# Performance work log

Hardware: AMD Instinct MI355X
Metric: run time of the kernel (lower is better)

## Reference

```python
import jax, jax.numpy as jnp
import numpy as np

N, NFEAT, NHID, NCLASS, NHEADS = 4096, 512, 64, 40, 8
ALPHA = 0.2
NEG = -9e15


def setup_inputs() -> dict:
    key = jax.random.key(0)
    ks = jax.random.split(key, 6)
    x = jax.random.normal(ks[0], (N, NFEAT), dtype=jnp.float32)
    adj = jax.random.randint(ks[1], (2, N, N), 0, 2, dtype=jnp.int32)
    # Xavier-ish scaled params
    W1 = jax.random.normal(ks[2], (NHEADS, NFEAT, NHID), dtype=jnp.float32) * (1.0 / np.sqrt(NFEAT))
    a1 = jax.random.normal(ks[3], (NHEADS, 2, NHID), dtype=jnp.float32) * (1.0 / np.sqrt(2 * NHID))
    Wo = jax.random.normal(ks[4], (NHEADS * NHID, NCLASS), dtype=jnp.float32) * (1.0 / np.sqrt(NHEADS * NHID))
    ao = jax.random.normal(ks[5], (2, NCLASS), dtype=jnp.float32) * (1.0 / np.sqrt(2 * NCLASS))
    return {"x": x, "adj": adj, "W1": W1, "a1": a1, "Wo": Wo, "ao": ao}


def _gat_layer(h, adj_mask, W, a_src, a_dst, concat):
    # h: [N,F]; W: [...,F,F']; a_src/a_dst: [...,F']
    if W.ndim == 3:  # multi-head: [H,F,F']
        Wh = jnp.einsum('nf,hfd->hnd', h, W)              # [H,N,F']
        f1 = jnp.einsum('hnd,hd->hn', Wh, a_src)           # [H,N]
        f2 = jnp.einsum('hnd,hd->hn', Wh, a_dst)
        e = jax.nn.leaky_relu(f1[:, :, None] + f2[:, None, :], ALPHA)  # [H,N,N]
        e = jnp.where(adj_mask[None], e, NEG)
        att = jax.nn.softmax(e, axis=-1)
        out = jnp.einsum('hnm,hmd->hnd', att, Wh)          # [H,N,F']
    else:
        Wh = h @ W                                         # [N,F']
        f1 = Wh @ a_src
        f2 = Wh @ a_dst
        e = jax.nn.leaky_relu(f1[:, None] + f2[None, :], ALPHA)
        e = jnp.where(adj_mask, e, NEG)
        att = jax.nn.softmax(e, axis=-1)
        out = att @ Wh
    return jax.nn.elu(out) if concat else out


def reference(x, adj, W1, a1, Wo, ao):
    adj1 = adj[1] > 0
    adj0 = adj[0] > 0
    # layer 1: NHEADS heads, concat=True
    h = _gat_layer(x, adj1, W1, a1[:, 0], a1[:, 1], concat=True)   # [H,N,NHID]
    h = jnp.transpose(h, (1, 0, 2)).reshape(x.shape[0], -1)        # [N, H*NHID]
    # output layer: concat=False, then outer ELU + log_softmax
    out = _gat_layer(h, adj0, Wo, ao[0], ao[1], concat=False)      # [N, NCLASS]
    out = jax.nn.elu(out)
    return jax.nn.log_softmax(out, axis=1)
```

## Files before the change

### kernel.cpp

```cpp
#include <hip/hip_runtime.h>
#include <hip/hip_bf16.h>

#define N      4096
#define NFEAT  512
#define NHID   64
#define NHEADS 8
#define NCLASS 40
#define ALPHA  0.2f
#define LOG2E  1.44269504f

typedef unsigned short u16;
typedef unsigned int   u32;
typedef __attribute__((ext_vector_type(8))) short bf16x8;
typedef __attribute__((ext_vector_type(4))) float f32x4;

__device__ __forceinline__ float b2f(u16 u) {
    return __uint_as_float(((u32)u) << 16);
}
__device__ __forceinline__ u32 rnd_hi(float f) {
    u32 u = __float_as_uint(f);
    return u + 0x7FFFu + ((u >> 16) & 1u);
}
__device__ __forceinline__ u32 pk2(float lo, float hi) {
    __hip_bfloat162 h = __float22bfloat162_rn(make_float2(lo, hi));
    return *(u32*)&h;
}
__device__ __forceinline__ u16 f2b(float f) {
    return (u16)(rnd_hi(f) >> 16);
}
__device__ __forceinline__ float mexp(int m, float t) {
    return m ? __builtin_amdgcn_exp2f(fmaxf(t, ALPHA * t)) : 0.f;
}
__device__ __forceinline__ bf16x8 ones_frag() {
    union { u16 u[8]; bf16x8 v; } o;
    #pragma unroll
    for (int j = 0; j < 8; ++j) o.u[j] = 0x3F80;
    return o.v;
}
__device__ __forceinline__ void gload_lds16(const u16* g, u16* l) {
    __builtin_amdgcn_global_load_lds(
        (const __attribute__((address_space(1))) void*)g,
        (__attribute__((address_space(3))) void*)l,
        16, 0, 0);
}

__global__ __launch_bounds__(256) void kcx(const float* __restrict__ x,
                                           u16* __restrict__ xb) {
    const int g = blockIdx.x * 256 + threadIdx.x;
    const size_t base = (size_t)g * 8;
    float4 v0 = *(const float4*)&x[base];
    float4 v1 = *(const float4*)&x[base + 4];
    uint4 o;
    o.x = pk2(v0.x, v0.y); o.y = pk2(v0.z, v0.w);
    o.z = pk2(v1.x, v1.y); o.w = pk2(v1.z, v1.w);
    *(uint4*)&xb[base] = o;
}

__global__ __launch_bounds__(256) void kcw(const float* __restrict__ W1,
                                           u16* __restrict__ W1b) {
    __shared__ float ts[64 * 68];
    const int t  = threadIdx.x;
    const int f0 = blockIdx.x * 64;
    const int h  = blockIdx.y;
    #pragma unroll
    for (int i = 0; i < 4; ++i) {
        int flat = t + 256 * i;
        int row = flat >> 4;
        int c4  = (flat & 15) * 4;
        *(float4*)&ts[row * 68 + c4] =
            *(const float4*)&W1[((size_t)h * 512 + f0 + row) * 64 + c4];
    }
    __syncthreads();
    const int d  = t >> 2;
    const int fs = (t & 3) * 16;
    u32 p[8];
    #pragma unroll
    for (int j = 0; j < 8; ++j)
        p[j] = pk2(ts[(fs + 2 * j) * 68 + d], ts[(fs + 2 * j + 1) * 68 + d]);
    u32* dst = (u32*)&W1b[((size_t)(h * 64 + d)) * 512 + f0 + fs];
    *(uint4*)dst       = make_uint4(p[0], p[1], p[2], p[3]);
    *(uint4*)(dst + 4) = make_uint4(p[4], p[5], p[6], p[7]);
}

__global__ __launch_bounds__(256, 4) void k1m_gemm1(const u16* __restrict__ xb,
                                                    const u16* __restrict__ W1b,
                                                    const float* __restrict__ a1,
                                                    u16* __restrict__ Wh1T,
                                                    float* __restrict__ F1,
                                                    float* __restrict__ F2) {
    __shared__ u16 xs[64 * 72];
    __shared__ u16 wvs[64 * 72];
    const int t    = threadIdx.x;
    const int n0   = blockIdx.x * 64;
    const int h    = blockIdx.y;
    const int lane = t & 63;
    const int l15  = lane & 15;
    const int q    = lane >> 4;
    const int wrow = (t >> 6) * 16;
    f32x4 acc[4];
    #pragma unroll
    for (int df = 0; df < 4; ++df)
        #pragma unroll
        for (int r = 0; r < 4; ++r) acc[df][r] = 0.f;
    for (int f0 = 0; f0 < 512; f0 += 64) {
        uint4 sx[2], sw[2];
        #pragma unroll
        for (int i = 0; i < 2; ++i) {
            int flat = t + 256 * i;
            int row = flat >> 3;
            int c8  = (flat & 7) * 8;
            sx[i] = *(const uint4*)&xb[(size_t)(n0 + row) * 512 + f0 + c8];
            sw[i] = *(const uint4*)&W1b[((size_t)(h * 64 + row)) * 512 + f0 + c8];
        }
        __syncthreads();
        #pragma unroll
        for (int i = 0; i < 2; ++i) {
            int flat = t + 256 * i;
            int row = flat >> 3;
            int c8  = (flat & 7) * 8;
            *(uint4*)&xs[row * 72 + c8]  = sx[i];
            *(uint4*)&wvs[row * 72 + c8] = sw[i];
        }
        __syncthreads();
        #pragma unroll
        for (int ks = 0; ks < 2; ++ks) {
            int k0 = ks * 32 + q * 8;
            bf16x8 a = *(const bf16x8*)&xs[(wrow + l15) * 72 + k0];
            #pragma unroll
            for (int df = 0; df < 4; ++df) {
                bf16x8 b = *(const bf16x8*)&wvs[(df * 16 + l15) * 72 + k0];
                acc[df] = __builtin_amdgcn_mfma_f32_16x16x32_bf16(a, b, acc[df], 0, 0, 0);
            }
        }
    }
    #pragma unroll
    for (int df = 0; df < 4; ++df) {
        uint2 o;
        o.x = pk2(acc[df][0], acc[df][1]);
        o.y = pk2(acc[df][2], acc[df][3]);
        *(uint2*)&Wh1T[((size_t)(h * 64 + df * 16 + l15)) * 4096 + n0 + wrow + q * 4] = o;
    }
    float a1v[4], a2v[4];
    #pragma unroll
    for (int df = 0; df < 4; ++df) {
        a1v[df] = a1[h * 128 + df * 16 + l15];
        a2v[df] = a1[h * 128 + 64 + df * 16 + l15];
    }
    #pragma unroll
    for (int r = 0; r < 4; ++r) {
        float s1 = 0.f, s2 = 0.f;
        #pragma unroll
        for (int df = 0; df < 4; ++df) {
            s1 += acc[df][r] * a1v[df];
            s2 += acc[df][r] * a2v[df];
        }
        #pragma unroll
        for (int off = 8; off >= 1; off >>= 1) {
            s1 += __shfl_xor(s1, off);
            s2 += __shfl_xor(s2, off);
        }
        if (l15 == 0) {
            int n = n0 + wrow + q * 4 + r;
            F1[h * 4096 + n] = s1 * LOG2E;
            F2[h * 4096 + n] = s2 * LOG2E;
        }
    }
}

__global__ __launch_bounds__(256, 4) void k3_attn1(const int* __restrict__ adj1,
                                                   const u16* __restrict__ Wh1T,
                                                   const float* __restrict__ F1,
                                                   const float* __restrict__ F2,
                                                   float* __restrict__ h1) {
    __shared__ __align__(16) u16 wbf[64 * 136];
    __shared__ __align__(16) u16 whT[64 * 128];
    __shared__ float f1s[64];
    const int t     = threadIdx.x;
    const int n0    = blockIdx.x * 64;
    const int h     = blockIdx.y;
    const int lane  = t & 63;
    const int l15   = lane & 15;
    const int q     = lane >> 4;
    const int wrow  = (t >> 6) * 16;
    const int c4    = (t & 31) * 4;
    const int rg    = t >> 5;
    const bf16x8 bones = ones_frag();
    if (t < 64) f1s[t] = F1[h * N + n0 + t];

    const int wv   = t >> 6;
    const int lsub = lane >> 4;
    const int slot = lane & 15;
    const u16* gsrc[4];
    #pragma unroll
    for (int i = 0; i < 4; ++i) {
        int row_l = wv * 16 + i * 4 + lsub;
        int sc    = (slot ^ ((i * 4 + lsub) & 7)) * 8;
        gsrc[i] = Wh1T + ((size_t)(h * 64 + row_l)) * 4096 + sc;
    }
    u16* ldst = &whT[wv * 2048];
    const int xb7 = l15 & 7;

    f32x4 acc[5];
    #pragma unroll
    for (int df = 0; df < 5; ++df)
        #pragma unroll
        for (int r = 0; r < 4; ++r) acc[df][r] = 0.f;

    int4 aprev[8];
    #pragma unroll
    for (int i = 0; i < 8; ++i)
        aprev[i] = *(const int4*)&adj1[(size_t)(n0 + rg + 8 * i) * N + c4];
    float4 f2n = *(const float4*)&F2[h * N + c4];
    __syncthreads();

    for (int m0 = 0; m0 < 4096; m0 += 128) {
        #pragma unroll
        for (int i = 0; i < 4; ++i)
            gload_lds16(gsrc[i] + m0, ldst + i * 512);
        const float4 F2v = f2n;
        const int mn = (m0 + 128 < 4096) ? m0 + 128 : 0;
        f2n = *(const float4*)&F2[h * N + mn + c4];
        #pragma unroll
        for (int i = 0; i < 8; ++i) {
            const int rr = rg + 8 * i;
            int4 a4 = aprev[i];
            aprev[i] = *(const int4*)&adj1[(size_t)(n0 + rr) * N + mn + c4];
            float f1v = f1s[rr];
            float w0 = mexp(a4.x, f1v + F2v.x);
            float w1 = mexp(a4.y, f1v + F2v.y);
            float w2 = mexp(a4.z, f1v + F2v.z);
            float w3 = mexp(a4.w, f1v + F2v.w);
            uint2 pk;
            pk.x = pk2(w0, w1);
            pk.y = pk2(w2, w3);
            *(uint2*)&wbf[rr * 136 + c4] = pk;
        }
        __syncthreads();
        #pragma unroll
        for (int ks = 0; ks < 4; ++ks) {
            int k0 = ks * 32 + q * 8;
            bf16x8 a = *(const bf16x8*)&wbf[(wrow + l15) * 136 + k0];
            #pragma unroll
            for (int df = 0; df < 4; ++df) {
                bf16x8 b = *(const bf16x8*)
                    &whT[(df * 16 + l15) * 128 + (((ks * 4 + q) ^ xb7) * 8)];
                acc[df] = __builtin_amdgcn_mfma_f32_16x16x32_bf16(a, b, acc[df], 0, 0, 0);
            }
            acc[4] = __builtin_amdgcn_mfma_f32_16x16x32_bf16(a, bones, acc[4], 0, 0, 0);
        }
        __syncthreads();
    }
    #pragma unroll
    for (int r = 0; r < 4; ++r) {
        const int nl = wrow + q * 4 + r;
        const float z = fmaxf(acc[4][r], 1e-30f);
        #pragma unroll
        for (int df = 0; df < 4; ++df) {
            float v = acc[df][r] / z;
            v = v > 0.f ? v : __expf(v) - 1.f;
            h1[(size_t)(n0 + nl) * 512 + h * 64 + df * 16 + l15] = v;
        }
    }
}

__global__ __launch_bounds__(256) void k4_gemm2(const float* __restrict__ h1,
                                                const float* __restrict__ Wo,
                                                const float* __restrict__ ao,
                                                float* __restrict__ F1o,
                                                float* __restrict__ F2o,
                                                u16* __restrict__ Wh2T) {
    const int t = threadIdx.x;
    const int c = t & 63;
    const int n = blockIdx.x * 4 + (t >> 6);
    float acc = 0.f;
    if (c < NCLASS) {
        const float* hrow = &h1[(size_t)n * 512];
        #pragma unroll 8
        for (int f = 0; f < 512; ++f)
            acc += hrow[f] * Wo[f * NCLASS + c];
        Wh2T[(size_t)c * 4096 + n] = f2b(acc);
    }
    float s1 = (c < NCLASS) ? acc * ao[c] : 0.f;
    float s2 = (c < NCLASS) ? acc * ao[NCLASS + c] : 0.f;
    #pragma unroll
    for (int off = 32; off >= 1; off >>= 1) {
        s1 += __shfl_xor(s1, off);
        s2 += __shfl_xor(s2, off);
    }
    if (c == 0) {
        F1o[n] = s1 * LOG2E;
        F2o[n] = s2 * LOG2E;
    }
}

__global__ __launch_bounds__(256, 4) void k5a_attn2(const int* __restrict__ adj0,
                                                    const u16* __restrict__ Wh2T,
                                                    const float* __restrict__ F1o,
                                                    const float* __restrict__ F2o,
                                                    float* __restrict__ pacc,
                                                    float* __restrict__ pz) {
    __shared__ __align__(16) u16 wbf[64 * 136];
    __shared__ __align__(16) u16 whT[48 * 128];
    __shared__ float f1s[64];
    const int t     = threadIdx.x;
    const int n0    = blockIdx.x * 64;
    const int chunk = blockIdx.y;
    const int mbase = chunk * 256;
    const int lane  = t & 63;
    const int l15   = lane & 15;
    const int q     = lane >> 4;
    const int wrow  = (t >> 6) * 16;
    const int c4    = (t & 31) * 4;
    const int rg    = t >> 5;
    const bf16x8 bones = ones_frag();
    if (t < 64) f1s[t] = F1o[n0 + t];
    #pragma unroll
    for (int i = 0; i < 4; ++i)
        whT[40 * 128 + t + 256 * i] = 0;

    const int wv   = t >> 6;
    const int lsub = lane >> 4;
    const int slot = lane & 15;
    const int ninst = (wv < 2) ? 4 : ((wv == 2) ? 2 : 0);
    const u16* gsrc[4];
    #pragma unroll
    for (int i = 0; i < 4; ++i) {
        int row_l = wv * 16 + i * 4 + lsub;
        int rl    = (row_l < 40) ? row_l : 0;
        int sc    = (slot ^ ((i * 4 + lsub) & 7)) * 8;
        gsrc[i] = Wh2T + (size_t)rl * 4096 + sc;
    }
    u16* ldst = &whT[wv * 2048];
    const int xb7 = l15 & 7;

    f32x4 acc[4];
    #pragma unroll
    for (int df = 0; df < 4; ++df)
        #pragma unroll
        for (int r = 0; r < 4; ++r) acc[df][r] = 0.f;

    int4 aprev[8];
    #pragma unroll
    for (int i = 0; i < 8; ++i)
        aprev[i] = *(const int4*)&adj0[(size_t)(n0 + rg + 8 * i) * N + mbase + c4];
    float4 f2n = *(const float4*)&F2o[mbase + c4];
    __syncthreads();

    #pragma unroll
    for (int mt = 0; mt < 2; ++mt) {
        const int m0 = mbase + mt * 128;
        #pragma unroll
        for (int i = 0; i < 4; ++i)
            if (i < ninst)
                gload_lds16(gsrc[i] + m0, ldst + i * 512);
        const float4 F2v = f2n;
        const int mn = mbase + ((mt + 1) & 1) * 128;
        f2n = *(const float4*)&F2o[mn + c4];
        #pragma unroll
        for (int i = 0; i < 8; ++i) {
            const int rr = rg + 8 * i;
            int4 a4 = aprev[i];
            aprev[i] = *(const int4*)&adj0[(size_t)(n0 + rr) * N + mn + c4];
            float f1v = f1s[rr];
            float w0 = mexp(a4.x, f1v + F2v.x);
            float w1 = mexp(a4.y, f1v + F2v.y);
            float w2 = mexp(a4.z, f1v + F2v.z);
            float w3 = mexp(a4.w, f1v + F2v.w);
            uint2 pk;
            pk.x = pk2(w0, w1);
            pk.y = pk2(w2, w3);
            *(uint2*)&wbf[rr * 136 + c4] = pk;
        }
        __syncthreads();
        #pragma unroll
        for (int ks = 0; ks < 4; ++ks) {
            int k0 = ks * 32 + q * 8;
            bf16x8 a = *(const bf16x8*)&wbf[(wrow + l15) * 136 + k0];
            #pragma unroll
            for (int df = 0; df < 3; ++df) {
                bf16x8 b = *(const bf16x8*)
                    &whT[(df * 16 + l15) * 128 + (((ks * 4 + q) ^ xb7) * 8)];
                acc[df] = __builtin_amdgcn_mfma_f32_16x16x32_bf16(a, b, acc[df], 0, 0, 0);
            }
            acc[3] = __builtin_amdgcn_mfma_f32_16x16x32_bf16(a, bones, acc[3], 0, 0, 0);
        }
        __syncthreads();
    }
    #pragma unroll
    for (int r = 0; r < 4; ++r) {
        int n = n0 + wrow + q * 4 + r;
        if (l15 == 0) pz[(size_t)chunk * N + n] = acc[3][r];
        #pragma unroll
        for (int df = 0; df < 3; ++df) {
            int c = df * 16 + l15;
            if (c < NCLASS)
                pacc[((size_t)chunk * N + n) * NCLASS + c] = acc[df][r];
        }
    }
}

__global__ __launch_bounds__(256) void k5b_final(const float* __restrict__ pacc,
                                                 const float* __restrict__ pz,
                                                 float* __restrict__ out) {
    const int t = threadIdx.x;
    const int lane = t & 63;
    const int n = blockIdx.x * 4 + (t >> 6);
    float s = 0.f, Z = 0.f;
    #pragma unroll
    for (int ch = 0; ch < 16; ++ch) {
        Z += pz[(size_t)ch * N + n];
        if (lane < NCLASS) s += pacc[(size_t)(ch * N + n) * NCLASS + lane];
    }
    float v;
    if (lane < NCLASS) {
        v = s / fmaxf(Z, 1e-30f);
        v = v > 0.f ? v : __expf(v) - 1.f;
    } else {
        v = -INFINITY;
    }
    float mx = v;
    #pragma unroll
    for (int off = 32; off >= 1; off >>= 1) mx = fmaxf(mx, __shfl_xor(mx, off));
    float ex = (lane < NCLASS) ? __expf(v - mx) : 0.f;
    #pragma unroll
    for (int off = 32; off >= 1; off >>= 1) ex += __shfl_xor(ex, off);
    float lse = mx + __logf(ex);
    if (lane < NCLASS) out[(size_t)n * NCLASS + lane] = v - lse;
}

extern "C" void kernel_launch(void* const* d_in, const int* in_sizes, int n_in,
                              void* d_out, int out_size, void* d_ws, size_t ws_size,
                              hipStream_t stream) {
    const float* x   = (const float*)d_in[0];
    const int*   adj = (const int*)d_in[1];
    const float* W1  = (const float*)d_in[2];
    const float* a1  = (const float*)d_in[3];
    const float* Wo  = (const float*)d_in[4];
    const float* ao  = (const float*)d_in[5];

    float* ws    = (float*)d_ws;
    float* h1    = ws;
    float* F1    = h1 + 2097152;
    float* F2    = F1 + 32768;
    float* F1o   = F2 + 32768;
    float* F2o   = F1o + 4096;
    float* pz    = F2o + 4096;
    float* pz1   = pz + 65536;
    u16*   Wh1T  = (u16*)(pz1 + 65536);
    u16*   Wh2T  = Wh1T + 2097152;
    float* R     = (float*)(Wh2T + 163840);
    u16*   xb    = (u16*)R;
    u16*   W1b   = xb + 2097152;
    float* pacc  = R;

    const int* adj0 = adj;
    const int* adj1 = adj + (size_t)N * N;

    hipLaunchKernelGGL(kcx,       dim3(1024),   dim3(256), 0, stream, x, xb);
    hipLaunchKernelGGL(kcw,       dim3(8, 8),   dim3(256), 0, stream, W1, W1b);
    hipLaunchKernelGGL(k1m_gemm1, dim3(64, 8),  dim3(256), 0, stream, xb, W1b, a1, Wh1T, F1, F2);
    hipLaunchKernelGGL(k3_attn1,  dim3(64, 8),  dim3(256), 0, stream, adj1, Wh1T, F1, F2, h1);
    hipLaunchKernelGGL(k4_gemm2,  dim3(1024),   dim3(256), 0, stream, h1, Wo, ao, F1o, F2o, Wh2T);
    hipLaunchKernelGGL(k5a_attn2, dim3(64, 16), dim3(256), 0, stream, adj0, Wh2T, F1o, F2o, pacc, pz);
    hipLaunchKernelGGL(k5b_final, dim3(1024),   dim3(256), 0, stream, pacc, pz, (float*)d_out);
}
```

Before: 331.6 us.

## Halve attn1 row tile to 32 and split head dims across waves

The first attention kernel now processes 32 destination rows per block instead of 64. The four waves are split into two row groups by two column halves, and the softmax denominator is shared through LDS. This doubles the grid to 1024 blocks for better CU occupancy and halves per-thread adjacency prefetch registers, at the cost of loading the Wh tile twice as often overall. The attn2 kernel also moves its adjacency prefetch after the exp stage, drops the F2 prefetch, and raises launch bounds to 5 waves per SIMD.

```diff
diff --git a/kernel.cpp b/kernel.cpp
--- a/kernel.cpp
+++ b/kernel.cpp
@@ -172,22 +172,24 @@
                                                    const float* __restrict__ F1,
                                                    const float* __restrict__ F2,
                                                    float* __restrict__ h1) {
-    __shared__ __align__(16) u16 wbf[64 * 136];
+    __shared__ __align__(16) u16 wbf[32 * 136];
     __shared__ __align__(16) u16 whT[64 * 128];
-    __shared__ float f1s[64];
+    __shared__ float f1s[32];
+    __shared__ float zs[32];
     const int t     = threadIdx.x;
-    const int n0    = blockIdx.x * 64;
+    const int n0    = blockIdx.x * 32;
     const int h     = blockIdx.y;
     const int lane  = t & 63;
     const int l15   = lane & 15;
     const int q     = lane >> 4;
-    const int wrow  = (t >> 6) * 16;
+    const int wv    = t >> 6;
+    const int rb    = (wv & 1) * 16;
+    const int dh    = wv >> 1;
     const int c4    = (t & 31) * 4;
     const int rg    = t >> 5;
     const bf16x8 bones = ones_frag();
-    if (t < 64) f1s[t] = F1[h * N + n0 + t];
-
-    const int wv   = t >> 6;
+    if (t < 32) f1s[t] = F1[h * N + n0 + t];
+
     const int lsub = lane >> 4;
     const int slot = lane & 15;
     const u16* gsrc[4];
@@ -200,15 +202,17 @@
     u16* ldst = &whT[wv * 2048];
     const int xb7 = l15 & 7;
 
-    f32x4 acc[5];
-    #pragma unroll
-    for (int df = 0; df < 5; ++df)
-        #pragma unroll
-        for (int r = 0; r < 4; ++r) acc[df][r] = 0.f;
-
-    int4 aprev[8];
-    #pragma unroll
-    for (int i = 0; i < 8; ++i)
+    f32x4 accd[2], accz;
+    #pragma unroll
+    for (int j = 0; j < 2; ++j)
+        #pragma unroll
+        for (int r = 0; r < 4; ++r) accd[j][r] = 0.f;
+    #pragma unroll
+    for (int r = 0; r < 4; ++r) accz[r] = 0.f;
+
+    int4 aprev[4];
+    #pragma unroll
+    for (int i = 0; i < 4; ++i)
         aprev[i] = *(const int4*)&adj1[(size_t)(n0 + rg + 8 * i) * N + c4];
     float4 f2n = *(const float4*)&F2[h * N + c4];
     __syncthreads();
@@ -221,7 +225,7 @@
         const int mn = (m0 + 128 < 4096) ? m0 + 128 : 0;
         f2n = *(const float4*)&F2[h * N + mn + c4];
         #pragma unroll
-        for (int i = 0; i < 8; ++i) {
+        for (int i = 0; i < 4; ++i) {
             const int rr = rg + 8 * i;
             int4 a4 = aprev[i];
             aprev[i] = *(const int4*)&adj1[(size_t)(n0 + rr) * N + mn + c4];
@@ -239,26 +243,33 @@
         #pragma unroll
         for (int ks = 0; ks < 4; ++ks) {
             int k0 = ks * 32 + q * 8;
-            bf16x8 a = *(const bf16x8*)&wbf[(wrow + l15) * 136 + k0];
+            bf16x8 a = *(const bf16x8*)&wbf[(rb + l15) * 136 + k0];
             #pragma unroll
-            for (int df = 0; df < 4; ++df) {
+            for (int j = 0; j < 2; ++j) {
+                const int df = dh * 2 + j;
                 bf16x8 b = *(const bf16x8*)
                     &whT[(df * 16 + l15) * 128 + (((ks * 4 + q) ^ xb7) * 8)];
-                acc[df] = __builtin_amdgcn_mfma_f32_16x16x32_bf16(a, b, acc[df], 0, 0, 0);
+                accd[j] = __builtin_amdgcn_mfma_f32_16x16x32_bf16(a, b, accd[j], 0, 0, 0);
             }
-            acc[4] = __builtin_amdgcn_mfma_f32_16x16x32_bf16(a, bones, acc[4], 0, 0, 0);
-        }
-        __syncthreads();
-    }
+            if (dh == 0)
+                accz = __builtin_amdgcn_mfma_f32_16x16x32_bf16(a, bones, accz, 0, 0, 0);
+        }
+        __syncthreads();
+    }
+    if (dh == 0 && l15 == 0) {
+        #pragma unroll
+        for (int r = 0; r < 4; ++r) zs[rb + q * 4 + r] = accz[r];
+    }
+    __syncthreads();
     #pragma unroll
     for (int r = 0; r < 4; ++r) {
-        const int nl = wrow + q * 4 + r;
-        const float z = fmaxf(acc[4][r], 1e-30f);
-        #pragma unroll
-        for (int df = 0; df < 4; ++df) {
-            float v = acc[df][r] / z;
+        const int nl = rb + q * 4 + r;
+        const float z = fmaxf(zs[nl], 1e-30f);
+        #pragma unroll
+        for (int j = 0; j < 2; ++j) {
+            float v = accd[j][r] / z;
             v = v > 0.f ? v : __expf(v) - 1.f;
-            h1[(size_t)(n0 + nl) * 512 + h * 64 + df * 16 + l15] = v;
+            h1[(size_t)(n0 + nl) * 512 + h * 64 + (dh * 2 + j) * 16 + l15] = v;
         }
     }
 }
@@ -293,7 +304,7 @@
     }
 }
 
-__global__ __launch_bounds__(256, 4) void k5a_attn2(const int* __restrict__ adj0,
+__global__ __launch_bounds__(256, 5) void k5a_attn2(const int* __restrict__ adj0,
                                                     const u16* __restrict__ Wh2T,
                                                     const float* __restrict__ F1o,
                                                     const float* __restrict__ F2o,
@@ -343,7 +354,6 @@
     #pragma unroll
     for (int i = 0; i < 8; ++i)
         aprev[i] = *(const int4*)&adj0[(size_t)(n0 + rg + 8 * i) * N + mbase + c4];
-    float4 f2n = *(const float4*)&F2o[mbase + c4];
     __syncthreads();
 
     #pragma unroll
@@ -353,14 +363,11 @@
         for (int i = 0; i < 4; ++i)
             if (i < ninst)
                 gload_lds16(gsrc[i] + m0, ldst + i * 512);
-        const float4 F2v = f2n;
-        const int mn = mbase + ((mt + 1) & 1) * 128;
-        f2n = *(const float4*)&F2o[mn + c4];
+        float4 F2v = *(const float4*)&F2o[m0 + c4];
         #pragma unroll
         for (int i = 0; i < 8; ++i) {
-            const int rr = rg + 8 * i;
+            int rr = rg + 8 * i;
             int4 a4 = aprev[i];
-            aprev[i] = *(const int4*)&adj0[(size_t)(n0 + rr) * N + mn + c4];
             float f1v = f1s[rr];
             float w0 = mexp(a4.x, f1v + F2v.x);
             float w1 = mexp(a4.y, f1v + F2v.y);
@@ -371,6 +378,10 @@
             pk.y = pk2(w2, w3);
             *(uint2*)&wbf[rr * 136 + c4] = pk;
         }
+        int mn = mbase + ((mt + 1) & 1) * 128;
+        #pragma unroll
+        for (int i = 0; i < 8; ++i)
+            aprev[i] = *(const int4*)&adj0[(size_t)(n0 + rg + 8 * i) * N + mn + c4];
         __syncthreads();
         #pragma unroll
         for (int ks = 0; ks < 4; ++ks) {
@@ -459,7 +470,7 @@
     hipLaunchKernelGGL(kcx,       dim3(1024),   dim3(256), 0, stream, x, xb);
     hipLaunchKernelGGL(kcw,       dim3(8, 8),   dim3(256), 0, stream, W1, W1b);
     hipLaunchKernelGGL(k1m_gemm1, dim3(64, 8),  dim3(256), 0, stream, xb, W1b, a1, Wh1T, F1, F2);
-    hipLaunchKernelGGL(k3_attn1,  dim3(64, 8),  dim3(256), 0, stream, adj1, Wh1T, F1, F2, h1);
+    hipLaunchKernelGGL(k3_attn1,  dim3(128, 8), dim3(256), 0, stream, adj1, Wh1T, F1, F2, h1);
     hipLaunchKernelGGL(k4_gemm2,  dim3(1024),   dim3(256), 0, stream, h1, Wo, ao, F1o, F2o, Wh2T);
     hipLaunchKernelGGL(k5a_attn2, dim3(64, 16), dim3(256), 0, stream, adj0, Wh2T, F1o, F2o, pacc, pz);
     hipLaunchKernelGGL(k5b_final, dim3(1024),   dim3(256), 0, stream, pacc, pz, (float*)d_out);
```

Result: faster. 318.7 us (-3.9%).
